# Optimization experiments

Hardware: AMD Instinct MI355X
Metric: run time of the kernel (lower is better)

The kernel has to match this reference:

```python
import jax, jax.numpy as jnp
import numpy as np

N_NODES = 50000
N_EDGES = 800000
DIM_FEAT = 96
INFO_DIM = 32
DIM_EMB = 160
CONV_OUT = DIM_EMB - INFO_DIM  # 128
NUM_LAYERS = 3
NUM_GRAPHS = 500
DIM_TARGET = 10


def setup_inputs() -> dict:
    key = jax.random.key(0)
    ks = jax.random.split(key, 20)
    inp = {
        'x': jax.random.normal(ks[0], (N_NODES, DIM_FEAT), dtype=jnp.float32),
        'edge_index': jax.random.randint(ks[1], (2, N_EDGES), 0, N_NODES, dtype=jnp.int32),
        'batch': jnp.sort(jax.random.randint(ks[2], (N_NODES,), 0, NUM_GRAPHS, dtype=jnp.int32)),
        'struc_info': jax.random.normal(ks[3], (NUM_GRAPHS, INFO_DIM), dtype=jnp.float32),
    }
    # SAGEConv params per layer: lin_l (on aggregated neighbors, with bias), lin_r (on root, no bias)
    in_dims = [DIM_FEAT + INFO_DIM, DIM_EMB, DIM_EMB]
    k = 4
    for i, din in enumerate(in_dims):
        s = 1.0 / np.sqrt(din)
        inp[f'Wl{i}'] = jax.random.uniform(ks[k], (din, CONV_OUT), jnp.float32, -s, s); k += 1
        inp[f'Wr{i}'] = jax.random.uniform(ks[k], (din, CONV_OUT), jnp.float32, -s, s); k += 1
        inp[f'b{i}'] = jax.random.uniform(ks[k], (CONV_OUT,), jnp.float32, -s, s); k += 1
    s1 = 1.0 / np.sqrt(NUM_LAYERS * CONV_OUT)
    inp['Wfc1'] = jax.random.uniform(ks[k], (NUM_LAYERS * CONV_OUT, DIM_EMB), jnp.float32, -s1, s1); k += 1
    inp['bfc1'] = jax.random.uniform(ks[k], (DIM_EMB,), jnp.float32, -s1, s1); k += 1
    s2 = 1.0 / np.sqrt(DIM_EMB)
    inp['Wfc2'] = jax.random.uniform(ks[k], (DIM_EMB, DIM_TARGET), jnp.float32, -s2, s2); k += 1
    inp['bfc2'] = jax.random.uniform(ks[k], (DIM_TARGET,), jnp.float32, -s2, s2)
    return inp


def _sage_conv(h, src, dst, Wl, Wr, b, n_nodes):
    # PyG SAGEConv (mean aggr): out = lin_l(mean_{j in N(i)} x_j) + lin_r(x_i)
    agg = jax.ops.segment_sum(h[src], dst, num_segments=n_nodes)       # [N, D]
    deg = jax.ops.segment_sum(jnp.ones_like(dst, dtype=h.dtype), dst, num_segments=n_nodes)
    mean = agg / jnp.maximum(deg, 1.0)[:, None]
    return mean @ Wl + b + h @ Wr


def reference(x, edge_index, batch, struc_info, Wl0, Wr0, b0, Wl1, Wr1, b1, Wl2, Wr2, b2, Wfc1, bfc1, Wfc2, bfc2):
    n_nodes = x.shape[0]
    src, dst = edge_index[0], edge_index[1]
    info = struc_info[batch]                         # [N, info_dim] repeated per node
    params = [(Wl0, Wr0, b0), (Wl1, Wr1, b1), (Wl2, Wr2, b2)]
    h = x
    outs = []
    for (Wl, Wr, b) in params:
        h = _sage_conv(jnp.concatenate([h, info], axis=1), src, dst, Wl, Wr, b, n_nodes)
        outs.append(h)
    hcat = jnp.concatenate(outs, axis=1)             # [N, num_layers*conv_out]
    g = jax.ops.segment_max(hcat, batch, num_segments=struc_info.shape[0])  # global max pool
    z = jax.nn.relu(g @ Wfc1 + bfc1)
    return z @ Wfc2 + bfc2
```

## Files before the change

### kernel.cpp

```cpp
#include <hip/hip_runtime.h>
#include <hip/hip_bf16.h>
#include <float.h>

#define NN 50000
#define NE 800000
#define DF 96
#define DI 32
#define CO 128
#define NG 500
#define HC 384
#define F1I 384
#define F1O 160
#define F2O 10
#define NBLK 196

typedef unsigned int  u32;
typedef unsigned short u16;
typedef short bf16x8 __attribute__((ext_vector_type(8)));
typedef float f32x4  __attribute__((ext_vector_type(4)));

__device__ __forceinline__ u16 f2b(float f) {
    __hip_bfloat16 h = __float2bfloat16(f);
    return *reinterpret_cast<u16*>(&h);
}
__device__ __forceinline__ float b2f(u16 u) {
    return __uint_as_float(((u32)u) << 16);
}
__device__ __forceinline__ float blo(u32 u) { return __uint_as_float(u << 16); }
__device__ __forceinline__ float bhi(u32 u) { return __uint_as_float(u & 0xffff0000u); }

#define PB_CNT    196
#define PB_STARTS 196
#define PB_CAST   4688
#define PB_WT0    96
#define PB_WT1    128
#define PB_WT2    128
#define PB_INFO   500
#define PREP_GRID (PB_CNT + PB_STARTS + PB_CAST + PB_WT0 + PB_WT1 + PB_WT2 + 3 * PB_INFO)

__global__ __launch_bounds__(256) void k_prep(
        const float* __restrict__ x, const int* __restrict__ batch, const float* __restrict__ info,
        const float* __restrict__ Wl0, const float* __restrict__ Wr0, const float* __restrict__ b0,
        const float* __restrict__ Wl1, const float* __restrict__ Wr1, const float* __restrict__ b1,
        const float* __restrict__ Wl2, const float* __restrict__ Wr2, const float* __restrict__ b2,
        int* __restrict__ cnt, int* __restrict__ start, u16* __restrict__ xb,
        u16* __restrict__ WT0, u16* __restrict__ WT1, u16* __restrict__ WT2,
        float* __restrict__ iQl0, float* __restrict__ iQr0,
        float* __restrict__ iQl1, float* __restrict__ iQr1,
        float* __restrict__ iQl2, float* __restrict__ iQr2) {
    int blk = blockIdx.x;
    int t = threadIdx.x;
    if (blk < PB_CNT) {
        int i = blk * 256 + t;
        if (i < NN) cnt[i] = 0;
        return;
    }
    blk -= PB_CNT;
    if (blk < PB_STARTS) {
        int i = blk * 256 + t;
        if (i >= NN) return;
        int b = batch[i];
        if (i == 0) { for (int g = 0; g <= b; ++g) start[g] = 0; }
        else {
            int p = batch[i - 1];
            if (p != b) for (int g = p + 1; g <= b; ++g) start[g] = i;
        }
        if (i == NN - 1) { for (int g = b + 1; g <= NG; ++g) start[g] = NN; }
        return;
    }
    blk -= PB_STARTS;
    if (blk < PB_CAST) {
        int tid = blk * 256 + t;
        if (tid >= NN * DF / 4) return;
        float4 v = *(const float4*)&x[tid * 4];
        ushort4 o;
        o.x = f2b(v.x); o.y = f2b(v.y); o.z = f2b(v.z); o.w = f2b(v.w);
        *(ushort4*)&xb[tid * 4] = o;
        return;
    }
    blk -= PB_CAST;
    if (blk < PB_WT0 + PB_WT1 + PB_WT2) {
        const float* Wl; const float* Wr; u16* WT; int K; int rel;
        if (blk < PB_WT0) { Wl = Wl0; Wr = Wr0; WT = WT0; K = 96;  rel = blk; }
        else if (blk < PB_WT0 + PB_WT1) { Wl = Wl1; Wr = Wr1; WT = WT1; K = 128; rel = blk - PB_WT0; }
        else { Wl = Wl2; Wr = Wr2; WT = WT2; K = 128; rel = blk - PB_WT0 - PB_WT1; }
        int tid = rel * 256 + t;
        if (tid >= 256 * K) return;
        int n = tid / K;
        int k = tid - n * K;
        float v = (n < CO) ? Wl[k * CO + n] : Wr[k * CO + (n - CO)];
        WT[tid] = f2b(v);
        return;
    }
    blk -= PB_WT0 + PB_WT1 + PB_WT2;
    {
        const float* Wl; const float* Wr; const float* bias; float* iQl; float* iQr; int Ktop; int g;
        if (blk < PB_INFO) { Wl = Wl0; Wr = Wr0; bias = b0; iQl = iQl0; iQr = iQr0; Ktop = 96;  g = blk; }
        else if (blk < 2 * PB_INFO) { Wl = Wl1; Wr = Wr1; bias = b1; iQl = iQl1; iQr = iQr1; Ktop = 128; g = blk - PB_INFO; }
        else { Wl = Wl2; Wr = Wr2; bias = b2; iQl = iQl2; iQr = iQr2; Ktop = 128; g = blk - 2 * PB_INFO; }
        int c = t & 127;
        int sel = t >> 7;
        const float* W = sel ? Wr : Wl;
        float a = sel ? bias[c] : 0.0f;
        for (int d = 0; d < DI; ++d)
            a += info[g * DI + d] * W[(Ktop + d) * CO + c];
        (sel ? iQr : iQl)[g * CO + c] = a;
    }
}

__global__ void k_hist(const int* __restrict__ dst, int* __restrict__ cnt) {
    int e = blockIdx.x * blockDim.x + threadIdx.x;
    if (e < NE) atomicAdd(&cnt[dst[e]], 1);
}

__global__ __launch_bounds__(256) void k_bsum(const int* __restrict__ cnt, int* __restrict__ bsum) {
    __shared__ int s[256];
    int i = blockIdx.x * 256 + threadIdx.x;
    s[threadIdx.x] = (i < NN) ? cnt[i] : 0;
    __syncthreads();
    for (int off = 128; off > 0; off >>= 1) {
        if (threadIdx.x < off) s[threadIdx.x] += s[threadIdx.x + off];
        __syncthreads();
    }
    if (threadIdx.x == 0) bsum[blockIdx.x] = s[0];
}

__global__ __launch_bounds__(256) void k_scanb(const int* __restrict__ bsum, int* __restrict__ bpre) {
    __shared__ int s[256];
    int tid = threadIdx.x;
    int v = (tid < NBLK) ? bsum[tid] : 0;
    s[tid] = v;
    __syncthreads();
    for (int off = 1; off < 256; off <<= 1) {
        int t = (tid >= off) ? s[tid - off] : 0;
        __syncthreads();
        s[tid] += t;
        __syncthreads();
    }
    if (tid < NBLK) bpre[tid] = s[tid] - v;
}

__global__ __launch_bounds__(256) void k_rowptr(const int* __restrict__ cnt, const int* __restrict__ bpre,
                                                int* __restrict__ rowptr, int* __restrict__ fillc) {
    __shared__ int s[256];
    int tid = threadIdx.x;
    int i = blockIdx.x * 256 + tid;
    int v = (i < NN) ? cnt[i] : 0;
    s[tid] = v;
    __syncthreads();
    for (int off = 1; off < 256; off <<= 1) {
        int t = (tid >= off) ? s[tid - off] : 0;
        __syncthreads();
        s[tid] += t;
        __syncthreads();
    }
    int pre = bpre[blockIdx.x] + s[tid] - v;
    if (i < NN) { rowptr[i] = pre; fillc[i] = 0; }
    if (i == NN - 1) rowptr[NN] = pre + v;
}

__global__ void k_fill(const int* __restrict__ src, const int* __restrict__ dst,
                       const int* __restrict__ rowptr, int* __restrict__ fillc,
                       u16* __restrict__ csr) {
    int e = blockIdx.x * blockDim.x + threadIdx.x;
    if (e >= NE) return;
    int d = dst[e];
    int p = atomicAdd(&fillc[d], 1);
    csr[rowptr[d] + p] = (u16)src[e];
}

template<int K>
__global__ __launch_bounds__(256) void k_mfma(const u16* __restrict__ A,
                                              const u16* __restrict__ WTg,
                                              const int* __restrict__ batch,
                                              const float* __restrict__ iQl,
                                              const float* __restrict__ iQr,
                                              u16* __restrict__ zlp,
                                              u16* __restrict__ zq) {
    constexpr int PITCH = K + 8;
    __shared__ short lds[256 * PITCH];

    int tid  = threadIdx.x;
    int w    = tid >> 6;
    int lane = tid & 63;
    int quad = lane >> 4;
    int l15  = lane & 15;

    constexpr int CH = 256 * K / 8;
    const uint4* wp = (const uint4*)WTg;
    for (int c = tid; c < CH; c += 256) {
        int n  = c / (K / 8);
        int ko = (c - n * (K / 8)) * 8;
        *(uint4*)&lds[n * PITCH + ko] = wp[c];
    }
    __syncthreads();

    int i0 = blockIdx.x * 128 + w * 32;
    int r0 = i0 + l15;       if (r0 >= NN) r0 = NN - 1;
    int r1 = i0 + 16 + l15;  if (r1 >= NN) r1 = NN - 1;
    const short* A0 = (const short*)A + (size_t)r0 * K;
    const short* A1 = (const short*)A + (size_t)r1 * K;

    f32x4 acc[2][16];
#pragma unroll
    for (int rt = 0; rt < 2; ++rt)
#pragma unroll
        for (int ct = 0; ct < 16; ++ct)
            acc[rt][ct] = (f32x4){0.f, 0.f, 0.f, 0.f};

#pragma unroll
    for (int ks = 0; ks < K / 32; ++ks) {
        int ka = ks * 32 + quad * 8;
        bf16x8 a0 = *(const bf16x8*)(A0 + ka);
        bf16x8 a1 = *(const bf16x8*)(A1 + ka);
#pragma unroll
        for (int ct = 0; ct < 16; ++ct) {
            bf16x8 b = *(const bf16x8*)&lds[(ct * 16 + l15) * PITCH + ka];
            acc[0][ct] = __builtin_amdgcn_mfma_f32_16x16x32_bf16(a0, b, acc[0][ct], 0, 0, 0);
            acc[1][ct] = __builtin_amdgcn_mfma_f32_16x16x32_bf16(a1, b, acc[1][ct], 0, 0, 0);
        }
    }

#pragma unroll
    for (int rt = 0; rt < 2; ++rt) {
#pragma unroll
        for (int reg = 0; reg < 4; ++reg) {
            int row = i0 + rt * 16 + quad * 4 + reg;
            if (row < NN) {
                int b = batch[row];
                const float* ql = &iQl[b * CO];
                const float* qr = &iQr[b * CO];
                u16* lp = zlp + (size_t)row * CO;
                u16* qp = zq  + (size_t)row * CO;
#pragma unroll
                for (int ct = 0; ct < 8; ++ct) {
                    int col = ct * 16 + l15;
                    lp[col] = f2b(acc[rt][ct][reg] + ql[col]);
                }
#pragma unroll
                for (int ct = 8; ct < 16; ++ct) {
                    int col = ct * 16 + l15 - 128;
                    qp[col] = f2b(acc[rt][ct][reg] + qr[col]);
                }
            }
        }
    }
}

__global__ __launch_bounds__(256) void k_gatherb(const u32* __restrict__ zlp, const u32* __restrict__ zq,
                                                 const int* __restrict__ rowptr, const u16* __restrict__ csr,
                                                 u32* __restrict__ hout) {
    int wave = threadIdx.x >> 6;
    int lane = threadIdx.x & 63;
    int i = blockIdx.x * 4 + wave;
    if (i >= NN) return;
    int s0 = rowptr[i], s1 = rowptr[i + 1];
    float a0 = 0.f, a1 = 0.f, b0 = 0.f, b1 = 0.f;
    float c0 = 0.f, c1 = 0.f, d0 = 0.f, d1 = 0.f;
    int e = s0;
    for (; e + 7 < s1; e += 8) {
        int sA = csr[e],     sB = csr[e + 1], sC = csr[e + 2], sD = csr[e + 3];
        int sE = csr[e + 4], sF = csr[e + 5], sG = csr[e + 6], sH = csr[e + 7];
        u32 uA = zlp[sA * 64 + lane];
        u32 uB = zlp[sB * 64 + lane];
        u32 uC = zlp[sC * 64 + lane];
        u32 uD = zlp[sD * 64 + lane];
        u32 uE = zlp[sE * 64 + lane];
        u32 uF = zlp[sF * 64 + lane];
        u32 uG = zlp[sG * 64 + lane];
        u32 uH = zlp[sH * 64 + lane];
        a0 += blo(uA) + blo(uB); a1 += bhi(uA) + bhi(uB);
        b0 += blo(uC) + blo(uD); b1 += bhi(uC) + bhi(uD);
        c0 += blo(uE) + blo(uF); c1 += bhi(uE) + bhi(uF);
        d0 += blo(uG) + blo(uH); d1 += bhi(uG) + bhi(uH);
    }
    for (; e + 1 < s1; e += 2) {
        int sA = csr[e], sB = csr[e + 1];
        u32 uA = zlp[sA * 64 + lane];
        u32 uB = zlp[sB * 64 + lane];
        a0 += blo(uA) + blo(uB); a1 += bhi(uA) + bhi(uB);
    }
    if (e < s1) {
        u32 uA = zlp[csr[e] * 64 + lane];
        a0 += blo(uA); a1 += bhi(uA);
    }
    a0 += b0 + c0 + d0;
    a1 += b1 + c1 + d1;
    float r = 1.0f / fmaxf((float)(s1 - s0), 1.0f);
    u32 q = zq[i * 64 + lane];
    float h0 = a0 * r + blo(q);
    float h1 = a1 * r + bhi(q);
    hout[i * 64 + lane] = (u32)f2b(h0) | ((u32)f2b(h1) << 16);
}

__global__ __launch_bounds__(384) void k_poolfc(const u16* __restrict__ h1, const u16* __restrict__ h2,
                                                const u16* __restrict__ h3, const int* __restrict__ start,
                                                const float* __restrict__ W1, const float* __restrict__ b1,
                                                const float* __restrict__ W2, const float* __restrict__ b2,
                                                float* __restrict__ out) {
    __shared__ float s_g[F1I];
    __shared__ float s_z[F1O];
    int gr = blockIdx.x;
    int c  = threadIdx.x;
    int sel = c >> 7;
    int cc  = c & 127;
    const u16* hb = (sel == 0) ? h1 : (sel == 1) ? h2 : h3;
    int s = start[gr], e = start[gr + 1];
    float m0 = -FLT_MAX, m1 = -FLT_MAX;
    int n = s;
    for (; n + 1 < e; n += 2) {
        m0 = fmaxf(m0, b2f(hb[n * 128 + cc]));
        m1 = fmaxf(m1, b2f(hb[(n + 1) * 128 + cc]));
    }
    if (n < e) m0 = fmaxf(m0, b2f(hb[n * 128 + cc]));
    s_g[c] = fmaxf(m0, m1);
    __syncthreads();
    if (c < F1O) {
        float acc = b1[c];
        for (int k = 0; k < F1I; ++k) acc += s_g[k] * W1[k * F1O + c];
        s_z[c] = fmaxf(acc, 0.0f);
    }
    __syncthreads();
    if (c < F2O) {
        float a = b2[c];
        for (int k = 0; k < F1O; ++k) a += s_z[k] * W2[k * F2O + c];
        out[gr * F2O + c] = a;
    }
}

extern "C" void kernel_launch(void* const* d_in, const int* in_sizes, int n_in,
                              void* d_out, int out_size, void* d_ws, size_t ws_size,
                              hipStream_t stream) {
    const float* x     = (const float*)d_in[0];
    const int*   eidx  = (const int*)d_in[1];
    const int*   batch = (const int*)d_in[2];
    const float* info  = (const float*)d_in[3];
    const float* Wl0 = (const float*)d_in[4];
    const float* Wr0 = (const float*)d_in[5];
    const float* b0  = (const float*)d_in[6];
    const float* Wl1 = (const float*)d_in[7];
    const float* Wr1 = (const float*)d_in[8];
    const float* b1  = (const float*)d_in[9];
    const float* Wl2 = (const float*)d_in[10];
    const float* Wr2 = (const float*)d_in[11];
    const float* b2  = (const float*)d_in[12];
    const float* Wfc1  = (const float*)d_in[13];
    const float* bfc1  = (const float*)d_in[14];
    const float* Wfc2  = (const float*)d_in[15];
    const float* bfc2  = (const float*)d_in[16];
    float* out = (float*)d_out;

    const int* src = eidx;
    const int* dst = eidx + NE;

    char* W = (char*)d_ws;
    u16* xb     = (u16*)(W + 0);
    u16* h1     = (u16*)(W + 9600000);
    u16* h2     = (u16*)(W + 22400000);
    u16* h3     = (u16*)(W + 35200000);
    u16* zlp    = (u16*)(W + 48000000);
    u16* zq     = (u16*)(W + 60800000);
    u16* WT0    = (u16*)(W + 73600000);
    u16* WT1    = (u16*)(W + 73649152);
    u16* WT2    = (u16*)(W + 73714688);
    float* iQl0 = (float*)(W + 73780224);
    float* iQr0 = (float*)(W + 74036224);
    float* iQl1 = (float*)(W + 74292224);
    float* iQr1 = (float*)(W + 74548224);
    float* iQl2 = (float*)(W + 74804224);
    float* iQr2 = (float*)(W + 75060224);
    int* start  = (int*)(W + 75316224);
    int* rowptr = (int*)(W + 75318272);
    int* cnt    = (int*)(W + 75518336);
    int* fillc  = (int*)(W + 75718336);
    u16* csr    = (u16*)(W + 75918336);
    int* bsum   = (int*)(W + 77518336);
    int* bpre   = (int*)(W + 77519360);

    k_prep<<<PREP_GRID, 256, 0, stream>>>(x, batch, info,
        Wl0, Wr0, b0, Wl1, Wr1, b1, Wl2, Wr2, b2,
        cnt, start, xb, WT0, WT1, WT2, iQl0, iQr0, iQl1, iQr1, iQl2, iQr2);

    k_hist<<<(NE + 255) / 256, 256, 0, stream>>>(dst, cnt);
    k_bsum<<<NBLK, 256, 0, stream>>>(cnt, bsum);
    k_scanb<<<1, 256, 0, stream>>>(bsum, bpre);
    k_rowptr<<<NBLK, 256, 0, stream>>>(cnt, bpre, rowptr, fillc);
    k_fill<<<(NE + 255) / 256, 256, 0, stream>>>(src, dst, rowptr, fillc, csr);

    const int gGemm = (NN + 127) / 128;
    const int gGath = (NN + 3) / 4;

    k_mfma<96><<<gGemm, 256, 0, stream>>>(xb, WT0, batch, iQl0, iQr0, zlp, zq);
    k_gatherb<<<gGath, 256, 0, stream>>>((const u32*)zlp, (const u32*)zq, rowptr, csr, (u32*)h1);

    k_mfma<128><<<gGemm, 256, 0, stream>>>(h1, WT1, batch, iQl1, iQr1, zlp, zq);
    k_gatherb<<<gGath, 256, 0, stream>>>((const u32*)zlp, (const u32*)zq, rowptr, csr, (u32*)h2);

    k_mfma<128><<<gGemm, 256, 0, stream>>>(h2, WT2, batch, iQl2, iQr2, zlp, zq);
    k_gatherb<<<gGath, 256, 0, stream>>>((const u32*)zlp, (const u32*)zq, rowptr, csr, (u32*)h3);

    k_poolfc<<<NG, 384, 0, stream>>>(h1, h2, h3, start, Wfc1, bfc1, Wfc2, bfc2, out);
}
```

Measured before the change: 367.7 us.

## Partition CSR fill by XCD dst range and widen gather loads to 8 bytes

Result: no change. 367.7 us (-0.0%).

```diff
diff --git a/kernel.cpp b/kernel.cpp
--- a/kernel.cpp
+++ b/kernel.cpp
@@ -13,6 +13,7 @@
 #define F1O 160
 #define F2O 10
 #define NBLK 196
+#define DPX 6250
 
 typedef unsigned int  u32;
 typedef unsigned short u16;
@@ -159,14 +160,20 @@
     if (i == NN - 1) rowptr[NN] = pre + v;
 }
 
-__global__ void k_fill(const int* __restrict__ src, const int* __restrict__ dst,
-                       const int* __restrict__ rowptr, int* __restrict__ fillc,
-                       u16* __restrict__ csr) {
-    int e = blockIdx.x * blockDim.x + threadIdx.x;
+__global__ __launch_bounds__(256) void k_fill(const int* __restrict__ src, const int* __restrict__ dst,
+                                              const int* __restrict__ rowptr, int* __restrict__ fillc,
+                                              u16* __restrict__ csr) {
+    int xcd   = blockIdx.x & 7;
+    int chunk = blockIdx.x >> 3;
+    int lo = xcd * DPX;
+    int hi = lo + DPX;
+    int e = chunk * 256 + threadIdx.x;
     if (e >= NE) return;
     int d = dst[e];
-    int p = atomicAdd(&fillc[d], 1);
-    csr[rowptr[d] + p] = (u16)src[e];
+    if (d >= lo && d < hi) {
+        int p = atomicAdd(&fillc[d], 1);
+        csr[rowptr[d] + p] = (u16)src[e];
+    }
 }
 
 template<int K>
@@ -252,45 +259,60 @@
                                                  u32* __restrict__ hout) {
     int wave = threadIdx.x >> 6;
     int lane = threadIdx.x & 63;
+    int half = lane >> 5;
+    int l32  = lane & 31;
     int i = blockIdx.x * 4 + wave;
     if (i >= NN) return;
     int s0 = rowptr[i], s1 = rowptr[i + 1];
-    float a0 = 0.f, a1 = 0.f, b0 = 0.f, b1 = 0.f;
-    float c0 = 0.f, c1 = 0.f, d0 = 0.f, d1 = 0.f;
+    int deg = s1 - s0;
+
+    float a[4] = {0.f, 0.f, 0.f, 0.f};
+    float b[4] = {0.f, 0.f, 0.f, 0.f};
+    float c[4] = {0.f, 0.f, 0.f, 0.f};
+    float d[4] = {0.f, 0.f, 0.f, 0.f};
+
     int e = s0;
     for (; e + 7 < s1; e += 8) {
-        int sA = csr[e],     sB = csr[e + 1], sC = csr[e + 2], sD = csr[e + 3];
-        int sE = csr[e + 4], sF = csr[e + 5], sG = csr[e + 6], sH = csr[e + 7];
-        u32 uA = zlp[sA * 64 + lane];
-        u32 uB = zlp[sB * 64 + lane];
-        u32 uC = zlp[sC * 64 + lane];
-        u32 uD = zlp[sD * 64 + lane];
-        u32 uE = zlp[sE * 64 + lane];
-        u32 uF = zlp[sF * 64 + lane];
-        u32 uG = zlp[sG * 64 + lane];
-        u32 uH = zlp[sH * 64 + lane];
-        a0 += blo(uA) + blo(uB); a1 += bhi(uA) + bhi(uB);
-        b0 += blo(uC) + blo(uD); b1 += bhi(uC) + bhi(uD);
-        c0 += blo(uE) + blo(uF); c1 += bhi(uE) + bhi(uF);
-        d0 += blo(uG) + blo(uH); d1 += bhi(uG) + bhi(uH);
+        int n0 = csr[e + half];
+        int n1 = csr[e + 2 + half];
+        int n2 = csr[e + 4 + half];
+        int n3 = csr[e + 6 + half];
+        uint2 u0 = *(const uint2*)(zlp + n0 * 64 + l32 * 2);
+        uint2 u1 = *(const uint2*)(zlp + n1 * 64 + l32 * 2);
+        uint2 u2 = *(const uint2*)(zlp + n2 * 64 + l32 * 2);
+        uint2 u3 = *(const uint2*)(zlp + n3 * 64 + l32 * 2);
+        a[0] += blo(u0.x); a[1] += bhi(u0.x); a[2] += blo(u0.y); a[3] += bhi(u0.y);
+        b[0] += blo(u1.x); b[1] += bhi(u1.x); b[2] += blo(u1.y); b[3] += bhi(u1.y);
+        c[0] += blo(u2.x); c[1] += bhi(u2.x); c[2] += blo(u2.y); c[3] += bhi(u2.y);
+        d[0] += blo(u3.x); d[1] += bhi(u3.x); d[2] += blo(u3.y); d[3] += bhi(u3.y);
     }
     for (; e + 1 < s1; e += 2) {
-        int sA = csr[e], sB = csr[e + 1];
-        u32 uA = zlp[sA * 64 + lane];
-        u32 uB = zlp[sB * 64 + lane];
-        a0 += blo(uA) + blo(uB); a1 += bhi(uA) + bhi(uB);
-    }
-    if (e < s1) {
-        u32 uA = zlp[csr[e] * 64 + lane];
-        a0 += blo(uA); a1 += bhi(uA);
-    }
-    a0 += b0 + c0 + d0;
-    a1 += b1 + c1 + d1;
-    float r = 1.0f / fmaxf((float)(s1 - s0), 1.0f);
-    u32 q = zq[i * 64 + lane];
-    float h0 = a0 * r + blo(q);
-    float h1 = a1 * r + bhi(q);
-    hout[i * 64 + lane] = (u32)f2b(h0) | ((u32)f2b(h1) << 16);
+        int n0 = csr[e + half];
+        uint2 u0 = *(const uint2*)(zlp + n0 * 64 + l32 * 2);
+        a[0] += blo(u0.x); a[1] += bhi(u0.x); a[2] += blo(u0.y); a[3] += bhi(u0.y);
+    }
+    if (e < s1 && half == 0) {
+        int n0 = csr[e];
+        uint2 u0 = *(const uint2*)(zlp + n0 * 64 + l32 * 2);
+        a[0] += blo(u0.x); a[1] += bhi(u0.x); a[2] += blo(u0.y); a[3] += bhi(u0.y);
+    }
+#pragma unroll
+    for (int j = 0; j < 4; ++j) {
+        a[j] += b[j] + c[j] + d[j];
+        a[j] += __shfl_xor(a[j], 32);
+    }
+    if (half == 0) {
+        float r = 1.0f / fmaxf((float)deg, 1.0f);
+        uint2 q = *(const uint2*)(zq + i * 64 + l32 * 2);
+        float h0 = a[0] * r + blo(q.x);
+        float h1 = a[1] * r + bhi(q.x);
+        float h2 = a[2] * r + blo(q.y);
+        float h3 = a[3] * r + bhi(q.y);
+        uint2 o;
+        o.x = (u32)f2b(h0) | ((u32)f2b(h1) << 16);
+        o.y = (u32)f2b(h2) | ((u32)f2b(h3) << 16);
+        *(uint2*)(hout + i * 64 + l32 * 2) = o;
+    }
 }
 
 __global__ __launch_bounds__(384) void k_poolfc(const u16* __restrict__ h1, const u16* __restrict__ h2,
@@ -385,7 +407,7 @@
     k_bsum<<<NBLK, 256, 0, stream>>>(cnt, bsum);
     k_scanb<<<1, 256, 0, stream>>>(bsum, bpre);
     k_rowptr<<<NBLK, 256, 0, stream>>>(cnt, bpre, rowptr, fillc);
-    k_fill<<<(NE + 255) / 256, 256, 0, stream>>>(src, dst, rowptr, fillc, csr);
+    k_fill<<<((NE + 255) / 256) * 8, 256, 0, stream>>>(src, dst, rowptr, fillc, csr);
 
     const int gGemm = (NN + 127) / 128;
     const int gGath = (NN + 3) / 4;
```

## Bucket CSR fill per block with LDS atomics and widen gather loads

Applied to the files above, without the earlier changes.

Result: slower. 672.1 us (+82.8%).

```diff
diff --git a/kernel.cpp b/kernel.cpp
--- a/kernel.cpp
+++ b/kernel.cpp
@@ -141,7 +141,7 @@
 }
 
 __global__ __launch_bounds__(256) void k_rowptr(const int* __restrict__ cnt, const int* __restrict__ bpre,
-                                                int* __restrict__ rowptr, int* __restrict__ fillc) {
+                                                int* __restrict__ rowptr) {
     __shared__ int s[256];
     int tid = threadIdx.x;
     int i = blockIdx.x * 256 + tid;
@@ -155,18 +155,29 @@
         __syncthreads();
     }
     int pre = bpre[blockIdx.x] + s[tid] - v;
-    if (i < NN) { rowptr[i] = pre; fillc[i] = 0; }
+    if (i < NN) rowptr[i] = pre;
     if (i == NN - 1) rowptr[NN] = pre + v;
 }
 
-__global__ void k_fill(const int* __restrict__ src, const int* __restrict__ dst,
-                       const int* __restrict__ rowptr, int* __restrict__ fillc,
-                       u16* __restrict__ csr) {
-    int e = blockIdx.x * blockDim.x + threadIdx.x;
-    if (e >= NE) return;
-    int d = dst[e];
-    int p = atomicAdd(&fillc[d], 1);
-    csr[rowptr[d] + p] = (u16)src[e];
+__global__ __launch_bounds__(256) void k_fill(const int* __restrict__ src, const int* __restrict__ dst,
+                                              const int* __restrict__ rowptr, u16* __restrict__ csr) {
+    __shared__ int base[256];
+    __shared__ int cntl[256];
+    int lo = blockIdx.x * 256;
+    int t = threadIdx.x;
+    if (lo + t < NN) base[t] = rowptr[lo + t];
+    cntl[t] = 0;
+    __syncthreads();
+    const int4* d4 = (const int4*)dst;
+    for (int e4 = t; e4 < NE / 4; e4 += 256) {
+        int4 dv = d4[e4];
+        int e = e4 * 4;
+        int r0 = dv.x - lo, r1 = dv.y - lo, r2 = dv.z - lo, r3 = dv.w - lo;
+        if ((unsigned)r0 < 256u) { int p = atomicAdd(&cntl[r0], 1); csr[base[r0] + p] = (u16)src[e]; }
+        if ((unsigned)r1 < 256u) { int p = atomicAdd(&cntl[r1], 1); csr[base[r1] + p] = (u16)src[e + 1]; }
+        if ((unsigned)r2 < 256u) { int p = atomicAdd(&cntl[r2], 1); csr[base[r2] + p] = (u16)src[e + 2]; }
+        if ((unsigned)r3 < 256u) { int p = atomicAdd(&cntl[r3], 1); csr[base[r3] + p] = (u16)src[e + 3]; }
+    }
 }
 
 template<int K>
@@ -247,50 +258,67 @@
     }
 }
 
+__device__ __forceinline__ void acc8(float* a, const uint4& u) {
+    a[0] += blo(u.x); a[1] += bhi(u.x);
+    a[2] += blo(u.y); a[3] += bhi(u.y);
+    a[4] += blo(u.z); a[5] += bhi(u.z);
+    a[6] += blo(u.w); a[7] += bhi(u.w);
+}
+
 __global__ __launch_bounds__(256) void k_gatherb(const u32* __restrict__ zlp, const u32* __restrict__ zq,
                                                  const int* __restrict__ rowptr, const u16* __restrict__ csr,
                                                  u32* __restrict__ hout) {
     int wave = threadIdx.x >> 6;
     int lane = threadIdx.x & 63;
+    int q    = lane >> 4;
+    int l16  = lane & 15;
     int i = blockIdx.x * 4 + wave;
     if (i >= NN) return;
     int s0 = rowptr[i], s1 = rowptr[i + 1];
-    float a0 = 0.f, a1 = 0.f, b0 = 0.f, b1 = 0.f;
-    float c0 = 0.f, c1 = 0.f, d0 = 0.f, d1 = 0.f;
+    int deg = s1 - s0;
+
+    const uint4* Z = (const uint4*)zlp;
+
+    float a[8] = {0,0,0,0,0,0,0,0};
+    float b[8] = {0,0,0,0,0,0,0,0};
+    float c[8] = {0,0,0,0,0,0,0,0};
+    float d[8] = {0,0,0,0,0,0,0,0};
+
     int e = s0;
-    for (; e + 7 < s1; e += 8) {
-        int sA = csr[e],     sB = csr[e + 1], sC = csr[e + 2], sD = csr[e + 3];
-        int sE = csr[e + 4], sF = csr[e + 5], sG = csr[e + 6], sH = csr[e + 7];
-        u32 uA = zlp[sA * 64 + lane];
-        u32 uB = zlp[sB * 64 + lane];
-        u32 uC = zlp[sC * 64 + lane];
-        u32 uD = zlp[sD * 64 + lane];
-        u32 uE = zlp[sE * 64 + lane];
-        u32 uF = zlp[sF * 64 + lane];
-        u32 uG = zlp[sG * 64 + lane];
-        u32 uH = zlp[sH * 64 + lane];
-        a0 += blo(uA) + blo(uB); a1 += bhi(uA) + bhi(uB);
-        b0 += blo(uC) + blo(uD); b1 += bhi(uC) + bhi(uD);
-        c0 += blo(uE) + blo(uF); c1 += bhi(uE) + bhi(uF);
-        d0 += blo(uG) + blo(uH); d1 += bhi(uG) + bhi(uH);
-    }
-    for (; e + 1 < s1; e += 2) {
-        int sA = csr[e], sB = csr[e + 1];
-        u32 uA = zlp[sA * 64 + lane];
-        u32 uB = zlp[sB * 64 + lane];
-        a0 += blo(uA) + blo(uB); a1 += bhi(uA) + bhi(uB);
-    }
-    if (e < s1) {
-        u32 uA = zlp[csr[e] * 64 + lane];
-        a0 += blo(uA); a1 += bhi(uA);
-    }
-    a0 += b0 + c0 + d0;
-    a1 += b1 + c1 + d1;
-    float r = 1.0f / fmaxf((float)(s1 - s0), 1.0f);
-    u32 q = zq[i * 64 + lane];
-    float h0 = a0 * r + blo(q);
-    float h1 = a1 * r + bhi(q);
-    hout[i * 64 + lane] = (u32)f2b(h0) | ((u32)f2b(h1) << 16);
+    for (; e + 15 < s1; e += 16) {
+        int n0 = csr[e + q];
+        int n1 = csr[e + 4 + q];
+        int n2 = csr[e + 8 + q];
+        int n3 = csr[e + 12 + q];
+        uint4 u0 = Z[(size_t)n0 * 16 + l16];
+        uint4 u1 = Z[(size_t)n1 * 16 + l16];
+        uint4 u2 = Z[(size_t)n2 * 16 + l16];
+        uint4 u3 = Z[(size_t)n3 * 16 + l16];
+        acc8(a, u0); acc8(b, u1); acc8(c, u2); acc8(d, u3);
+    }
+    for (; e < s1; e += 4) {
+        if (e + q < s1) {
+            int n0 = csr[e + q];
+            uint4 u0 = Z[(size_t)n0 * 16 + l16];
+            acc8(a, u0);
+        }
+    }
+#pragma unroll
+    for (int j = 0; j < 8; ++j) {
+        a[j] += b[j] + c[j] + d[j];
+        a[j] += __shfl_xor(a[j], 16);
+        a[j] += __shfl_xor(a[j], 32);
+    }
+    if (q == 0) {
+        float r = 1.0f / fmaxf((float)deg, 1.0f);
+        uint4 qq = ((const uint4*)zq)[(size_t)i * 16 + l16];
+        uint4 o;
+        o.x = (u32)f2b(a[0] * r + blo(qq.x)) | ((u32)f2b(a[1] * r + bhi(qq.x)) << 16);
+        o.y = (u32)f2b(a[2] * r + blo(qq.y)) | ((u32)f2b(a[3] * r + bhi(qq.y)) << 16);
+        o.z = (u32)f2b(a[4] * r + blo(qq.z)) | ((u32)f2b(a[5] * r + bhi(qq.z)) << 16);
+        o.w = (u32)f2b(a[6] * r + blo(qq.w)) | ((u32)f2b(a[7] * r + bhi(qq.w)) << 16);
+        ((uint4*)hout)[(size_t)i * 16 + l16] = o;
+    }
 }
 
 __global__ __launch_bounds__(384) void k_poolfc(const u16* __restrict__ h1, const u16* __restrict__ h2,
@@ -372,10 +400,9 @@
     int* start  = (int*)(W + 75316224);
     int* rowptr = (int*)(W + 75318272);
     int* cnt    = (int*)(W + 75518336);
-    int* fillc  = (int*)(W + 75718336);
-    u16* csr    = (u16*)(W + 75918336);
-    int* bsum   = (int*)(W + 77518336);
-    int* bpre   = (int*)(W + 77519360);
+    u16* csr    = (u16*)(W + 75718336);
+    int* bsum   = (int*)(W + 77318336);
+    int* bpre   = (int*)(W + 77319360);
 
     k_prep<<<PREP_GRID, 256, 0, stream>>>(x, batch, info,
         Wl0, Wr0, b0, Wl1, Wr1, b1, Wl2, Wr2, b2,
@@ -384,8 +411,8 @@
     k_hist<<<(NE + 255) / 256, 256, 0, stream>>>(dst, cnt);
     k_bsum<<<NBLK, 256, 0, stream>>>(cnt, bsum);
     k_scanb<<<1, 256, 0, stream>>>(bsum, bpre);
-    k_rowptr<<<NBLK, 256, 0, stream>>>(cnt, bpre, rowptr, fillc);
-    k_fill<<<(NE + 255) / 256, 256, 0, stream>>>(src, dst, rowptr, fillc, csr);
+    k_rowptr<<<NBLK, 256, 0, stream>>>(cnt, bpre, rowptr);
+    k_fill<<<NBLK, 256, 0, stream>>>(src, dst, rowptr, csr);
 
     const int gGemm = (NN + 127) / 128;
     const int gGath = (NN + 3) / 4;
```
